# Performance work log

Measured on AMD Instinct MI355X. Metric: run time of the kernel, lower is better.

Reference implementation:

```python
import jax, jax.numpy as jnp
import numpy as np

NENTITY = 100000
NRELATION = 500
HIDDEN = 256
GAMMA = 12.0
BATCH = 8


def setup_inputs() -> dict:
    key = jax.random.key(0)
    k1, k2, k3, k4 = jax.random.split(key, 4)
    entity_embedding = jax.random.normal(k1, (NENTITY, HIDDEN), dtype=jnp.float32)
    relation_embedding = jax.random.normal(k2, (NRELATION, HIDDEN), dtype=jnp.float32)
    positive_sample = jax.random.randint(k3, (BATCH, 3), 0, NRELATION, dtype=jnp.int64)
    negative_sample = jax.random.randint(k4, (BATCH, NENTITY), 0, NENTITY, dtype=jnp.int64)
    return {
        "entity_embedding": entity_embedding,
        "relation_embedding": relation_embedding,
        "positive_sample": positive_sample,
        "negative_sample": negative_sample,
    }


def reference(entity_embedding, relation_embedding, positive_sample, negative_sample):
    # 'tail-batch' mode of KGEModel.forward + TransE scoring.
    # head, relation come from the positive triple; tail is every negative candidate.
    head = entity_embedding[positive_sample[:, 0]][:, None, :]      # [B, 1, H]
    relation = relation_embedding[positive_sample[:, 1]][:, None, :]  # [B, 1, H]
    tail = entity_embedding[negative_sample]                          # [B, N, H]
    # score = gamma - || head + relation - tail ||_1
    score = GAMMA - jnp.sum(jnp.abs(head + relation - tail), axis=-1)  # [B, N]
    return score
```

## Files before the change

### kernel.cpp

```cpp
#include <hip/hip_runtime.h>

#define HIDDEN 256
#define GAMMA_F 12.0f
#define BATCH 8

__global__ __launch_bounds__(256) void kge_dist_kernel(
    const float* __restrict__ ent,
    const float* __restrict__ rel,
    const int*  __restrict__ pos,
    float* __restrict__ dist,
    int nent)
{
    const int lane = threadIdx.x & 63;
    const int wave = threadIdx.x >> 6;
    const int e = blockIdx.x * 4 + wave;
    if (e >= nent) return;

    float4 hr[BATCH];
    #pragma unroll
    for (int b = 0; b < BATCH; ++b) {
        const int hidx = pos[b * 3 + 0];
        const int ridx = pos[b * 3 + 1];
        const float4 h4 = *(const float4*)(ent + (size_t)hidx * HIDDEN + lane * 4);
        const float4 r4 = *(const float4*)(rel + (size_t)ridx * HIDDEN + lane * 4);
        hr[b] = make_float4(h4.x + r4.x, h4.y + r4.y, h4.z + r4.z, h4.w + r4.w);
    }

    const float4 t4 = *(const float4*)(ent + (size_t)e * HIDDEN + lane * 4);

    float acc[BATCH];
    #pragma unroll
    for (int b = 0; b < BATCH; ++b) {
        acc[b] = fabsf(hr[b].x - t4.x) + fabsf(hr[b].y - t4.y)
               + fabsf(hr[b].z - t4.z) + fabsf(hr[b].w - t4.w);
    }

    float v[4];
    {
        const bool p = lane & 1;
        #pragma unroll
        for (int k = 0; k < 4; ++k) {
            const float keep = p ? acc[2 * k + 1] : acc[2 * k];
            const float give = p ? acc[2 * k]     : acc[2 * k + 1];
            v[k] = keep + __shfl_xor(give, 1, 64);
        }
    }
    float w2[2];
    {
        const bool p = (lane >> 1) & 1;
        #pragma unroll
        for (int k = 0; k < 2; ++k) {
            const float keep = p ? v[2 * k + 1] : v[2 * k];
            const float give = p ? v[2 * k]     : v[2 * k + 1];
            w2[k] = keep + __shfl_xor(give, 2, 64);
        }
    }
    float s;
    {
        const bool p = (lane >> 2) & 1;
        const float keep = p ? w2[1] : w2[0];
        const float give = p ? w2[0] : w2[1];
        s = keep + __shfl_xor(give, 4, 64);
    }
    s += __shfl_xor(s, 8, 64);
    s += __shfl_xor(s, 16, 64);
    s += __shfl_xor(s, 32, 64);

    if (lane < BATCH)
        dist[(size_t)e * BATCH + lane] = GAMMA_F - s;
}

__global__ __launch_bounds__(256) void kge_gather_kernel(
    const int*  __restrict__ neg,
    const float* __restrict__ dist,
    float* __restrict__ out,
    int nneg)
{
    const int b = blockIdx.y;
    const int n = blockIdx.x * 256 + threadIdx.x;
    if (n >= nneg) return;
    const size_t off = (size_t)b * nneg + n;
    out[off] = dist[(size_t)neg[off] * BATCH + b];
}

__global__ __launch_bounds__(256) void kge_transe_kernel(
    const float* __restrict__ ent,
    const float* __restrict__ rel,
    const int*  __restrict__ pos,
    const int*  __restrict__ neg,
    float* __restrict__ out,
    int nneg, int nchunks)
{
    const int b     = blockIdx.y;
    const int lane  = threadIdx.x & 63;
    const int wave  = threadIdx.x >> 6;
    const int chunk = blockIdx.x * 4 + wave;
    if (chunk >= nchunks) return;
    const int n0 = chunk * 64;

    const int hidx = pos[b * 3 + 0];
    const int ridx = pos[b * 3 + 1];
    const float4 h4 = *(const float4*)(ent + (size_t)hidx * HIDDEN + lane * 4);
    const float4 r4 = *(const float4*)(rel + (size_t)ridx * HIDDEN + lane * 4);
    const float4 hr = make_float4(h4.x + r4.x, h4.y + r4.y,
                                  h4.z + r4.z, h4.w + r4.w);

    const int n_lane = n0 + lane;
    const int myidx = (n_lane < nneg) ? neg[(size_t)b * nneg + n_lane] : 0;
    const int valid = (nneg - n0 < 64) ? (nneg - n0) : 64;
    float res = 0.0f;

    #pragma unroll 4
    for (int i = 0; i < 64; ++i) {
        if (i >= valid) break;
        const int t = __shfl(myidx, i, 64);
        const float4 t4 = *(const float4*)(ent + (size_t)t * HIDDEN + lane * 4);
        float s = fabsf(hr.x - t4.x) + fabsf(hr.y - t4.y)
                + fabsf(hr.z - t4.z) + fabsf(hr.w - t4.w);
        #pragma unroll
        for (int off = 1; off < 64; off <<= 1)
            s += __shfl_xor(s, off, 64);
        if (lane == i) res = GAMMA_F - s;
    }

    if (n_lane < nneg) out[(size_t)b * nneg + n_lane] = res;
}

extern "C" void kernel_launch(void* const* d_in, const int* in_sizes, int n_in,
                              void* d_out, int out_size, void* d_ws, size_t ws_size,
                              hipStream_t stream) {
    const float* ent = (const float*)d_in[0];
    const float* rel = (const float*)d_in[1];
    const int*   pos = (const int*)d_in[2];
    const int*   neg = (const int*)d_in[3];
    float* out = (float*)d_out;

    const int nent = in_sizes[0] / HIDDEN;
    const int nneg = in_sizes[3] / BATCH;
    const size_t dist_bytes = (size_t)nent * BATCH * sizeof(float);

    if (ws_size >= dist_bytes) {
        float* dist = (float*)d_ws;
        dim3 gridA((nent + 3) / 4);
        kge_dist_kernel<<<gridA, 256, 0, stream>>>(ent, rel, pos, dist, nent);
        dim3 gridB((nneg + 255) / 256, BATCH);
        kge_gather_kernel<<<gridB, 256, 0, stream>>>(neg, dist, out, nneg);
    } else {
        const int nchunks = (nneg + 63) / 64;
        dim3 grid((nchunks + 3) / 4, BATCH);
        kge_transe_kernel<<<grid, 256, 0, stream>>>(ent, rel, pos, neg, out,
                                                    nneg, nchunks);
    }
}
```

Measured before the change: 197.7 us.

## Use persistent grid-stride waves with 8-row batching in distance kernel and vectorized gather

The distance kernel now runs a fixed grid of 1024 blocks. Each wave loops over groups of 8 entity rows, loading all 8 rows before computing, so the h+r setup is amortized, more loads are in flight, and each wave writes 64 contiguous dist values per group. The gather kernel handles two negatives per thread using int2 index loads and float2 stores. The fallback path for small workspaces has been removed, so the code now assumes the workspace is always large enough for the dist table.

```diff
diff --git a/kernel.cpp b/kernel.cpp
--- a/kernel.cpp
+++ b/kernel.cpp
@@ -9,12 +9,11 @@
     const float* __restrict__ rel,
     const int*  __restrict__ pos,
     float* __restrict__ dist,
-    int nent)
+    int ngroups, int nent)
 {
     const int lane = threadIdx.x & 63;
-    const int wave = threadIdx.x >> 6;
-    const int e = blockIdx.x * 4 + wave;
-    if (e >= nent) return;
+    const int wave_gid = (blockIdx.x * 256 + threadIdx.x) >> 6;
+    const int nwaves = gridDim.x * 4;
 
     float4 hr[BATCH];
     #pragma unroll
@@ -26,48 +25,100 @@
         hr[b] = make_float4(h4.x + r4.x, h4.y + r4.y, h4.z + r4.z, h4.w + r4.w);
     }
 
-    const float4 t4 = *(const float4*)(ent + (size_t)e * HIDDEN + lane * 4);
+    for (int grp = wave_gid; grp < ngroups; grp += nwaves) {
+        const float* base = ent + (size_t)grp * 8 * HIDDEN + lane * 4;
 
-    float acc[BATCH];
-    #pragma unroll
-    for (int b = 0; b < BATCH; ++b) {
-        acc[b] = fabsf(hr[b].x - t4.x) + fabsf(hr[b].y - t4.y)
-               + fabsf(hr[b].z - t4.z) + fabsf(hr[b].w - t4.w);
+        float4 t[8];
+        #pragma unroll
+        for (int r = 0; r < 8; ++r)
+            t[r] = *(const float4*)(base + r * HIDDEN);
+
+        float res = 0.0f;
+        #pragma unroll
+        for (int r = 0; r < 8; ++r) {
+            float acc[BATCH];
+            #pragma unroll
+            for (int b = 0; b < BATCH; ++b) {
+                acc[b] = fabsf(hr[b].x - t[r].x) + fabsf(hr[b].y - t[r].y)
+                       + fabsf(hr[b].z - t[r].z) + fabsf(hr[b].w - t[r].w);
+            }
+            float v[4];
+            {
+                const bool p = lane & 1;
+                #pragma unroll
+                for (int k = 0; k < 4; ++k) {
+                    const float keep = p ? acc[2 * k + 1] : acc[2 * k];
+                    const float give = p ? acc[2 * k]     : acc[2 * k + 1];
+                    v[k] = keep + __shfl_xor(give, 1, 64);
+                }
+            }
+            float w2[2];
+            {
+                const bool p = (lane >> 1) & 1;
+                #pragma unroll
+                for (int k = 0; k < 2; ++k) {
+                    const float keep = p ? v[2 * k + 1] : v[2 * k];
+                    const float give = p ? v[2 * k]     : v[2 * k + 1];
+                    w2[k] = keep + __shfl_xor(give, 2, 64);
+                }
+            }
+            float s;
+            {
+                const bool p = (lane >> 2) & 1;
+                const float keep = p ? w2[1] : w2[0];
+                const float give = p ? w2[0] : w2[1];
+                s = keep + __shfl_xor(give, 4, 64);
+            }
+            s += __shfl_xor(s, 8, 64);
+            s += __shfl_xor(s, 16, 64);
+            s += __shfl_xor(s, 32, 64);
+            if ((lane >> 3) == r) res = GAMMA_F - s;
+        }
+        dist[(size_t)grp * 64 + lane] = res;
     }
 
-    float v[4];
-    {
-        const bool p = lane & 1;
-        #pragma unroll
-        for (int k = 0; k < 4; ++k) {
-            const float keep = p ? acc[2 * k + 1] : acc[2 * k];
-            const float give = p ? acc[2 * k]     : acc[2 * k + 1];
-            v[k] = keep + __shfl_xor(give, 1, 64);
+    if (wave_gid == 0) {
+        for (int e = ngroups * 8; e < nent; ++e) {
+            const float4 t4 = *(const float4*)(ent + (size_t)e * HIDDEN + lane * 4);
+            float acc[BATCH];
+            #pragma unroll
+            for (int b = 0; b < BATCH; ++b) {
+                acc[b] = fabsf(hr[b].x - t4.x) + fabsf(hr[b].y - t4.y)
+                       + fabsf(hr[b].z - t4.z) + fabsf(hr[b].w - t4.w);
+            }
+            float v[4];
+            {
+                const bool p = lane & 1;
+                #pragma unroll
+                for (int k = 0; k < 4; ++k) {
+                    const float keep = p ? acc[2 * k + 1] : acc[2 * k];
+                    const float give = p ? acc[2 * k]     : acc[2 * k + 1];
+                    v[k] = keep + __shfl_xor(give, 1, 64);
+                }
+            }
+            float w2[2];
+            {
+                const bool p = (lane >> 1) & 1;
+                #pragma unroll
+                for (int k = 0; k < 2; ++k) {
+                    const float keep = p ? v[2 * k + 1] : v[2 * k];
+                    const float give = p ? v[2 * k]     : v[2 * k + 1];
+                    w2[k] = keep + __shfl_xor(give, 2, 64);
+                }
+            }
+            float s;
+            {
+                const bool p = (lane >> 2) & 1;
+                const float keep = p ? w2[1] : w2[0];
+                const float give = p ? w2[0] : w2[1];
+                s = keep + __shfl_xor(give, 4, 64);
+            }
+            s += __shfl_xor(s, 8, 64);
+            s += __shfl_xor(s, 16, 64);
+            s += __shfl_xor(s, 32, 64);
+            if (lane < BATCH) dist[(size_t)e * BATCH + lane] = GAMMA_F - s;
         }
     }
-    float w2[2];
-    {
-        const bool p = (lane >> 1) & 1;
-        #pragma unroll
-        for (int k = 0; k < 2; ++k) {
-            const float keep = p ? v[2 * k + 1] : v[2 * k];
-            const float give = p ? v[2 * k]     : v[2 * k + 1];
-            w2[k] = keep + __shfl_xor(give, 2, 64);
-        }
-    }
-    float s;
-    {
-        const bool p = (lane >> 2) & 1;
-        const float keep = p ? w2[1] : w2[0];
-        const float give = p ? w2[0] : w2[1];
-        s = keep + __shfl_xor(give, 4, 64);
-    }
-    s += __shfl_xor(s, 8, 64);
-    s += __shfl_xor(s, 16, 64);
-    s += __shfl_xor(s, 32, 64);
-
-    if (lane < BATCH)
-        dist[(size_t)e * BATCH + lane] = GAMMA_F - s;
 }
 
 __global__ __launch_bounds__(256) void kge_gather_kernel(
@@ -77,53 +128,17 @@
     int nneg)
 {
     const int b = blockIdx.y;
-    const int n = blockIdx.x * 256 + threadIdx.x;
-    if (n >= nneg) return;
-    const size_t off = (size_t)b * nneg + n;
-    out[off] = dist[(size_t)neg[off] * BATCH + b];
-}
-
-__global__ __launch_bounds__(256) void kge_transe_kernel(
-    const float* __restrict__ ent,
-    const float* __restrict__ rel,
-    const int*  __restrict__ pos,
-    const int*  __restrict__ neg,
-    float* __restrict__ out,
-    int nneg, int nchunks)
-{
-    const int b     = blockIdx.y;
-    const int lane  = threadIdx.x & 63;
-    const int wave  = threadIdx.x >> 6;
-    const int chunk = blockIdx.x * 4 + wave;
-    if (chunk >= nchunks) return;
-    const int n0 = chunk * 64;
-
-    const int hidx = pos[b * 3 + 0];
-    const int ridx = pos[b * 3 + 1];
-    const float4 h4 = *(const float4*)(ent + (size_t)hidx * HIDDEN + lane * 4);
-    const float4 r4 = *(const float4*)(rel + (size_t)ridx * HIDDEN + lane * 4);
-    const float4 hr = make_float4(h4.x + r4.x, h4.y + r4.y,
-                                  h4.z + r4.z, h4.w + r4.w);
-
-    const int n_lane = n0 + lane;
-    const int myidx = (n_lane < nneg) ? neg[(size_t)b * nneg + n_lane] : 0;
-    const int valid = (nneg - n0 < 64) ? (nneg - n0) : 64;
-    float res = 0.0f;
-
-    #pragma unroll 4
-    for (int i = 0; i < 64; ++i) {
-        if (i >= valid) break;
-        const int t = __shfl(myidx, i, 64);
-        const float4 t4 = *(const float4*)(ent + (size_t)t * HIDDEN + lane * 4);
-        float s = fabsf(hr.x - t4.x) + fabsf(hr.y - t4.y)
-                + fabsf(hr.z - t4.z) + fabsf(hr.w - t4.w);
-        #pragma unroll
-        for (int off = 1; off < 64; off <<= 1)
-            s += __shfl_xor(s, off, 64);
-        if (lane == i) res = GAMMA_F - s;
+    const int n = (blockIdx.x * 256 + threadIdx.x) * 2;
+    if (n + 1 < nneg) {
+        const int2 idx = *(const int2*)(neg + (size_t)b * nneg + n);
+        float2 r;
+        r.x = dist[(size_t)idx.x * BATCH + b];
+        r.y = dist[(size_t)idx.y * BATCH + b];
+        *(float2*)(out + (size_t)b * nneg + n) = r;
+    } else if (n < nneg) {
+        out[(size_t)b * nneg + n] =
+            dist[(size_t)neg[(size_t)b * nneg + n] * BATCH + b];
     }
-
-    if (n_lane < nneg) out[(size_t)b * nneg + n_lane] = res;
 }
 
 extern "C" void kernel_launch(void* const* d_in, const int* in_sizes, int n_in,
@@ -137,18 +152,12 @@
 
     const int nent = in_sizes[0] / HIDDEN;
     const int nneg = in_sizes[3] / BATCH;
-    const size_t dist_bytes = (size_t)nent * BATCH * sizeof(float);
+    float* dist = (float*)d_ws;
 
-    if (ws_size >= dist_bytes) {
-        float* dist = (float*)d_ws;
-        dim3 gridA((nent + 3) / 4);
-        kge_dist_kernel<<<gridA, 256, 0, stream>>>(ent, rel, pos, dist, nent);
-        dim3 gridB((nneg + 255) / 256, BATCH);
-        kge_gather_kernel<<<gridB, 256, 0, stream>>>(neg, dist, out, nneg);
-    } else {
-        const int nchunks = (nneg + 63) / 64;
-        dim3 grid((nchunks + 3) / 4, BATCH);
-        kge_transe_kernel<<<grid, 256, 0, stream>>>(ent, rel, pos, neg, out,
-                                                    nneg, nchunks);
-    }
+    const int ngroups = nent / 8;
+    kge_dist_kernel<<<1024, 256, 0, stream>>>(ent, rel, pos, dist, ngroups, nent);
+
+    const int npairs = (nneg + 1) / 2;
+    dim3 gridB((npairs + 255) / 256, BATCH);
+    kge_gather_kernel<<<gridB, 256, 0, stream>>>(neg, dist, out, nneg);
 }
```

Measured after the change: 166.2 us. -15.9%, faster.
